# Kernel optimization log

Measured on AMD Instinct MI355X. Metric: run time of the kernel, lower is better.

## Reference

```python
import jax, jax.numpy as jnp
import numpy as np

B = 8192       # atmospheric columns (batch)
NLAY = 60      # vertical levels (RNN sequence length)
NX = 4         # per-level input features
NXS = 3        # surface scalar inputs
NH1 = 64       # rnn1 hidden
NH2 = 64       # rnn2 hidden
NMEM = 16      # latent memory width (nh_mem)
NY = 4         # per-level outputs
NYS = 3        # surface outputs


def _lstm(x, h0, c0, Wih, Whh, bih, bhh):
    """PyTorch-convention LSTM (gate order i,f,g,o). x: [B,T,nx] -> ([B,T,nh], hL, cL)."""
    b = bih + bhh
    WihT = Wih.T
    WhhT = Whh.T

    def step(carry, xt):
        h, c = carry
        g = xt @ WihT + h @ WhhT + b
        i, f, gg, o = jnp.split(g, 4, axis=-1)
        c = jax.nn.sigmoid(f) * c + jax.nn.sigmoid(i) * jnp.tanh(gg)
        h = jax.nn.sigmoid(o) * jnp.tanh(c)
        return (h, c), h

    (hL, cL), ys = jax.lax.scan(step, (h0, c0), jnp.swapaxes(x, 0, 1))
    return jnp.swapaxes(ys, 0, 1), hL, cL


def setup_inputs() -> dict:
    key = jax.random.key(0)
    ks = jax.random.split(key, 30)

    def p(i, shape):
        return jax.random.normal(ks[i], shape, jnp.float32) * 0.05

    return {
        "inputs_main": jax.random.normal(ks[0], (B, NLAY, NX), jnp.float32),
        "inputs_aux": jax.random.normal(ks[1], (B, NXS), jnp.float32),
        "rnn1_mem": jax.random.normal(ks[2], (B, NLAY, NMEM), jnp.float32),
        # mlp_initial: Linear(nx, nneur[0])
        "Wi": p(3, (NH1, NX)), "bi": p(4, (NH1,)),
        # mlp_surface1/2: Linear(nx_sfc, nh_rnn1)
        "Ws1": p(5, (NH1, NXS)), "bs1": p(6, (NH1,)),
        "Ws2": p(7, (NH1, NXS)), "bs2": p(8, (NH1,)),
        # mlp_toa1/2: Linear(1, nh_rnn2)
        "Wt1": p(9, (NH2, 1)), "bt1": p(10, (NH2,)),
        "Wt2": p(11, (NH2, 1)), "bt2": p(12, (NH2,)),
        # rnn1: LSTM(NH1+NMEM -> NH1)
        "Wih1": p(13, (4 * NH1, NH1 + NMEM)), "Whh1": p(14, (4 * NH1, NH1)),
        "bih1": p(15, (4 * NH1,)), "bhh1": p(16, (4 * NH1,)),
        # rnn2: LSTM(NH1 -> NH2)
        "Wih2": p(17, (4 * NH2, NH1)), "Whh2": p(18, (4 * NH2, NH2)),
        "bih2": p(19, (4 * NH2,)), "bhh2": p(20, (4 * NH2,)),
        # mlp_latent: Linear(NH2, NMEM)
        "Wl": p(21, (NMEM, NH2)), "bl": p(22, (NMEM,)),
        # mlp_output: Linear(NMEM, NY)
        "Wo": p(23, (NY, NMEM)), "bo": p(24, (NY,)),
        # mlp_surface_output: Linear(NH2, NYS)
        "Wso": p(25, (NYS, NH2)), "bso": p(26, (NYS,)),
    }


def reference(inputs_main, inputs_aux, rnn1_mem, Wi, bi, Ws1, bs1, Ws2, bs2,
              Wt1, bt1, Wt2, bt2, Wih1, Whh1, bih1, bhh1, Wih2, Whh2, bih2, bhh2,
              Wl, bl, Wo, bo, Wso, bso):
    # initial MLP + tanh
    x = jnp.tanh(inputs_main @ Wi.T + bi)                       # [B,L,NH1]
    # concat convective memory
    x = jnp.concatenate([x, rnn1_mem], axis=2)                  # [B,L,NH1+NMEM]
    # rnn1 runs surface->TOA: flip level axis
    x = jnp.flip(x, axis=1)
    hx = jnp.tanh(inputs_aux @ Ws1.T + bs1)                     # surface-conditioned h0
    cx = jnp.tanh(inputs_aux @ Ws2.T + bs2)
    r1, _, _ = _lstm(x, hx, cx, Wih1, Whh1, bih1, bhh1)
    r1 = jnp.flip(r1, axis=1)                                   # back to TOA->surface
    # rnn2 initialized from TOA scalar
    toa = inputs_aux[:, 1:2]
    hx2 = toa @ Wt1.T + bt1
    cx2 = toa @ Wt2.T + bt2
    r2, hL, _ = _lstm(r1, hx2, cx2, Wih2, Whh2, bih2, bhh2)     # [B,L,NH2]
    # intermediate latent MLP -> new per-level memory
    lat = r2 @ Wl.T + bl                                        # [B,L,NMEM]
    new_mem = lat
    out = lat @ Wo.T + bo                                       # [B,L,NY]
    out_sfc = hL @ Wso.T + bso                                  # [B,NYS]
    return (out, out_sfc, new_mem)
```

## Files before the change

kernel.cpp:

```cpp
#include <hip/hip_runtime.h>
#include <hip/hip_bf16.h>

#define BATCH 8192
#define NLAY  60
#define NH    64
#define NMEM  16
#define ROWS  16
#define TPB   256
#define S1    168
#define S2    136

typedef unsigned short ushort_t;
typedef __attribute__((ext_vector_type(8))) short short8;
typedef __attribute__((ext_vector_type(4))) short short4v;
typedef __attribute__((ext_vector_type(4))) float f32x4;
typedef __attribute__((ext_vector_type(4))) float f4v;

__device__ __forceinline__ float rcp_(float x) { return __builtin_amdgcn_rcpf(x); }
__device__ __forceinline__ float sigm_(float x) { return rcp_(1.0f + __expf(-x)); }
__device__ __forceinline__ float tanh_(float x) { return 1.0f - 2.0f * rcp_(__expf(2.0f * x) + 1.0f); }
__device__ __forceinline__ ushort_t f2bu(float f) {
  unsigned u = __float_as_uint(f);
  return (ushort_t)((u + 0x7FFFu + ((u >> 16) & 1u)) >> 16);
}
__device__ __forceinline__ float b2fu(ushort_t b) { return __uint_as_float(((unsigned)b) << 16); }

__device__ __forceinline__ f32x4 mfma16(short8 a, short8 b, f32x4 c) {
  return __builtin_amdgcn_mfma_f32_16x16x32_bf16(a, b, c, 0, 0, 0);
}

__global__ void wtranspose(const float* __restrict__ Wih1, const float* __restrict__ Whh1,
                           const float* __restrict__ Wih2, const float* __restrict__ Whh2,
                           const float* __restrict__ Wl, ushort_t* __restrict__ frag) {
  int e = blockIdx.x * 256 + threadIdx.x;
  float v;
  if (e < 40960) {
    int j = e & 7, lx = (e >> 3) & 63, rest = e >> 9;
    int ks = rest % 5, gw = rest / 5;
    int g = gw & 3, wv = gw >> 2;
    int uu = wv * 16 + (lx & 15);
    int k = ks * 32 + (lx >> 4) * 8 + j;
    int row = g * 64 + uu;
    v = (k < 80) ? Wih1[row * 80 + k] : (k < 144 ? Whh1[row * 64 + (k - 80)] : 0.0f);
  } else if (e < 73728) {
    int e2 = e - 40960;
    int j = e2 & 7, lx = (e2 >> 3) & 63, rest = e2 >> 9;
    int ks = rest & 3, g = (rest >> 2) & 3, wv = rest >> 4;
    int uu = wv * 16 + (lx & 15);
    int k = ks * 32 + (lx >> 4) * 8 + j;
    int row = g * 64 + uu;
    v = (k < 64) ? Wih2[row * 64 + k] : Whh2[row * 64 + (k - 64)];
  } else {
    int e3 = e - 73728;
    int j = e3 & 7, lx = (e3 >> 3) & 63, ks = e3 >> 9;
    int m = lx & 15, k = ks * 32 + (lx >> 4) * 8 + j;
    v = Wl[m * 64 + k];
  }
  frag[e] = f2bu(v);
}

__global__ __launch_bounds__(TPB, 2)
void lstm_fused(const float* __restrict__ inputs_main, const float* __restrict__ inputs_aux,
                const float* __restrict__ rnn1_mem,
                const float* __restrict__ Wi,  const float* __restrict__ bi,
                const float* __restrict__ Ws1, const float* __restrict__ bs1,
                const float* __restrict__ Ws2, const float* __restrict__ bs2,
                const float* __restrict__ Wt1, const float* __restrict__ bt1,
                const float* __restrict__ Wt2, const float* __restrict__ bt2,
                const float* __restrict__ bih1, const float* __restrict__ bhh1,
                const float* __restrict__ bih2, const float* __restrict__ bhh2,
                const float* __restrict__ bl,
                const ushort_t* __restrict__ W1f, const ushort_t* __restrict__ W2f,
                const ushort_t* __restrict__ Wlf_g,
                ushort_t* __restrict__ r1buf, ushort_t* __restrict__ hLbuf,
                float* __restrict__ new_mem) {
  __shared__ __align__(16) ushort_t xh1[16 * S1];
  __shared__ __align__(16) ushort_t xh2[16 * S2];
  __shared__ __align__(16) float inmS[16][244];

  const int tid = threadIdx.x;
  const int l  = tid & 63, w = tid >> 6;
  const int ln = l & 15,  lq = l >> 4;
  const int u  = w * 16 + ln;
  const int rowbase = lq * 4;
  const int b0 = blockIdx.x * ROWS;
  const int xr = tid >> 4, xm = tid & 15, xc0 = xm * 4;
  const int rr8 = tid >> 3, ch8 = tid & 7;

  short8 B1f[4][5];
#pragma unroll
  for (int g = 0; g < 4; ++g)
#pragma unroll
    for (int ks = 0; ks < 5; ++ks)
      B1f[g][ks] = *(const short8*)(W1f + (((w * 4 + g) * 5 + ks) << 9) + (l << 3));

  f4v wif[4];
#pragma unroll
  for (int cc = 0; cc < 4; ++cc) wif[cc] = *(const f4v*)(Wi + (xc0 + cc) * 4);
  f4v bifv = *(const f4v*)(bi + xc0);

  float bg1[4];
#pragma unroll
  for (int g = 0; g < 4; ++g) bg1[g] = bih1[g * 64 + u] + bhh1[g * 64 + u];

  for (int e = tid; e < 16 * 240; e += TPB) {
    int r = e / 240, c = e - r * 240;
    inmS[r][c] = inputs_main[(size_t)(b0 + r) * 240 + c];
  }
  if (tid < 192) {
    int r = tid / 12, cc2 = (tid - r * 12) * 2 + 144;
    xh1[r * S1 + cc2] = 0; xh1[r * S1 + cc2 + 1] = 0;
  }
  __syncthreads();

  float c1[4];
  {
    float mv = rnn1_mem[(size_t)(b0 + xr) * 960 + 59 * 16 + xm];
    xh1[xr * S1 + 64 + xm] = f2bu(mv);
    f4v xin = *(const f4v*)&inmS[xr][59 * 4];
    short4v xpv;
#pragma unroll
    for (int cc = 0; cc < 4; ++cc) {
      float a = bifv[cc] + wif[cc][0] * xin[0] + wif[cc][1] * xin[1] + wif[cc][2] * xin[2] + wif[cc][3] * xin[3];
      xpv[cc] = (short)f2bu(tanh_(a));
    }
    *(short4v*)&xh1[xr * S1 + xc0] = xpv;

    float w10 = Ws1[u * 3 + 0], w11 = Ws1[u * 3 + 1], w12 = Ws1[u * 3 + 2], bb1 = bs1[u];
    float w20 = Ws2[u * 3 + 0], w21 = Ws2[u * 3 + 1], w22 = Ws2[u * 3 + 2], bb2 = bs2[u];
#pragma unroll
    for (int reg = 0; reg < 4; ++reg) {
      int row = rowbase + reg;
      const float* ax = inputs_aux + (size_t)(b0 + row) * 3;
      float a0 = ax[0], a1 = ax[1], a2 = ax[2];
      xh1[row * S1 + 80 + u] = f2bu(tanh_(w10 * a0 + w11 * a1 + w12 * a2 + bb1));
      c1[reg] = tanh_(w20 * a0 + w21 * a1 + w22 * a2 + bb2);
    }
  }
  __syncthreads();

  for (int t = NLAY - 1; t >= 0; --t) {
    float mv = 0.0f; f4v xin = {};
    if (t > 0) {
      mv  = rnn1_mem[(size_t)(b0 + xr) * 960 + (t - 1) * 16 + xm];
      xin = *(const f4v*)&inmS[xr][(t - 1) * 4];
    }
    short8 af[5];
#pragma unroll
    for (int ks = 0; ks < 5; ++ks)
      af[ks] = *(const short8*)&xh1[ln * S1 + ks * 32 + lq * 8];
    short4v hv = {};
    if (t < 59) hv = *(const short4v*)&xh1[xr * S1 + 80 + xc0];

    f32x4 acc[4];
#pragma unroll
    for (int g = 0; g < 4; ++g) acc[g] = (f32x4){bg1[g], bg1[g], bg1[g], bg1[g]};
#pragma unroll
    for (int ks = 0; ks < 5; ++ks)
#pragma unroll
      for (int g = 0; g < 4; ++g) acc[g] = mfma16(af[ks], B1f[g][ks], acc[g]);

    if (t < 59)
      *(short4v*)(r1buf + ((size_t)(b0 + xr) * 60 + (t + 1)) * 64 + xc0) = hv;

    short4v xpv = {};
    if (t > 0) {
#pragma unroll
      for (int cc = 0; cc < 4; ++cc) {
        float a = bifv[cc] + wif[cc][0] * xin[0] + wif[cc][1] * xin[1] + wif[cc][2] * xin[2] + wif[cc][3] * xin[3];
        xpv[cc] = (short)f2bu(tanh_(a));
      }
    }
    ushort_t hu[4];
#pragma unroll
    for (int reg = 0; reg < 4; ++reg) {
      float ig = sigm_(acc[0][reg]);
      float fg = sigm_(acc[1][reg]);
      float gg = tanh_(acc[2][reg]);
      float og = sigm_(acc[3][reg]);
      float c  = fg * c1[reg] + ig * gg;
      c1[reg] = c;
      hu[reg] = f2bu(og * tanh_(c));
    }
    __syncthreads();
#pragma unroll
    for (int reg = 0; reg < 4; ++reg) xh1[(rowbase + reg) * S1 + 80 + u] = hu[reg];
    if (t > 0) {
      *(short4v*)&xh1[xr * S1 + xc0] = xpv;
      xh1[xr * S1 + 64 + xm] = f2bu(mv);
    }
    __syncthreads();
  }

  float c2[4], bg2[4], blv;
  short8 B2f[4][4], Wlf[2];
  {
    short4v hv = *(const short4v*)&xh1[xr * S1 + 80 + xc0];
    *(short4v*)(r1buf + ((size_t)(b0 + xr) * 60 + 0) * 64 + xc0) = hv;
    *(short4v*)&xh2[xr * S2 + xc0] = hv;

    float wt1u = Wt1[u], wt2u = Wt2[u], bt1u = bt1[u], bt2u = bt2[u];
#pragma unroll
    for (int reg = 0; reg < 4; ++reg) {
      int row = rowbase + reg;
      float toa = inputs_aux[(size_t)(b0 + row) * 3 + 1];
      xh2[row * S2 + 64 + u] = f2bu(toa * wt1u + bt1u);
      c2[reg] = toa * wt2u + bt2u;
    }
#pragma unroll
    for (int g = 0; g < 4; ++g) bg2[g] = bih2[g * 64 + u] + bhh2[g * 64 + u];
#pragma unroll
    for (int g = 0; g < 4; ++g)
#pragma unroll
      for (int ks = 0; ks < 4; ++ks)
        B2f[g][ks] = *(const short8*)(W2f + (((w * 4 + g) * 4 + ks) << 9) + (l << 3));
    Wlf[0] = *(const short8*)(Wlf_g + (l << 3));
    Wlf[1] = *(const short8*)(Wlf_g + 512 + (l << 3));
    blv = bl[ln];
  }
  __syncthreads();

  for (int t = 0; t < NLAY; ++t) {
    short8 r1v = {};
    if (t < 59 && tid < 128)
      r1v = *(const short8*)(r1buf + ((size_t)(b0 + rr8) * 60 + (t + 1)) * 64 + ch8 * 8);
    short8 af2[4];
#pragma unroll
    for (int ks = 0; ks < 4; ++ks)
      af2[ks] = *(const short8*)&xh2[ln * S2 + ks * 32 + lq * 8];

    f32x4 acc[4];
#pragma unroll
    for (int g = 0; g < 4; ++g) acc[g] = (f32x4){bg2[g], bg2[g], bg2[g], bg2[g]};
#pragma unroll
    for (int ks = 0; ks < 4; ++ks)
#pragma unroll
      for (int g = 0; g < 4; ++g) acc[g] = mfma16(af2[ks], B2f[g][ks], acc[g]);

    ushort_t h2u[4];
#pragma unroll
    for (int reg = 0; reg < 4; ++reg) {
      float ig = sigm_(acc[0][reg]);
      float fg = sigm_(acc[1][reg]);
      float gg = tanh_(acc[2][reg]);
      float og = sigm_(acc[3][reg]);
      float c  = fg * c2[reg] + ig * gg;
      c2[reg] = c;
      h2u[reg] = f2bu(og * tanh_(c));
    }
    __syncthreads();
#pragma unroll
    for (int reg = 0; reg < 4; ++reg) xh2[(rowbase + reg) * S2 + 64 + u] = h2u[reg];
    if (t < 59 && tid < 128)
      *(short8*)&xh2[rr8 * S2 + ch8 * 8] = r1v;
    __syncthreads();

    if (w == 0) {
      short8 afL0 = *(const short8*)&xh2[ln * S2 + 64 + lq * 8];
      short8 afL1 = *(const short8*)&xh2[ln * S2 + 64 + 32 + lq * 8];
      f32x4 accL = (f32x4){blv, blv, blv, blv};
      accL = mfma16(afL0, Wlf[0], accL);
      accL = mfma16(afL1, Wlf[1], accL);
#pragma unroll
      for (int reg = 0; reg < 4; ++reg)
        new_mem[((size_t)(b0 + rowbase + reg) * 60 + t) * 16 + ln] = accL[reg];
    }
  }

  {
    short4v hv = *(const short4v*)&xh2[xr * S2 + 64 + xc0];
    *(short4v*)(hLbuf + (size_t)(b0 + xr) * 64 + xc0) = hv;
  }
}

__global__ void postpass(const float* __restrict__ new_mem, const ushort_t* __restrict__ hLbuf,
                         const float* __restrict__ Wo, const float* __restrict__ bo,
                         const float* __restrict__ Wso, const float* __restrict__ bso,
                         float* __restrict__ out, float* __restrict__ out_sfc) {
  int idx = blockIdx.x * 256 + threadIdx.x;
  int b = idx / 60, t = idx - b * 60;
  f4v nm[4];
#pragma unroll
  for (int i = 0; i < 4; ++i) nm[i] = *(const f4v*)(new_mem + (size_t)idx * 16 + i * 4);
  f4v ov;
#pragma unroll
  for (int y = 0; y < 4; ++y) {
    float a = bo[y];
#pragma unroll
    for (int m = 0; m < 16; ++m) a += nm[m >> 2][m & 3] * Wo[y * 16 + m];
    ov[y] = a;
  }
  *(f4v*)(out + (size_t)idx * 4) = ov;

  if (t == 59) {
    const ushort_t* hp = hLbuf + (size_t)b * 64;
    float s0 = bso[0], s1 = bso[1], s2 = bso[2];
#pragma unroll
    for (int kk = 0; kk < 8; ++kk) {
      short8 v = *(const short8*)(hp + kk * 8);
#pragma unroll
      for (int j = 0; j < 8; ++j) {
        float h = b2fu((ushort_t)v[j]);
        int k = kk * 8 + j;
        s0 += h * Wso[0 * 64 + k];
        s1 += h * Wso[1 * 64 + k];
        s2 += h * Wso[2 * 64 + k];
      }
    }
    out_sfc[(size_t)b * 3 + 0] = s0;
    out_sfc[(size_t)b * 3 + 1] = s1;
    out_sfc[(size_t)b * 3 + 2] = s2;
  }
}

extern "C" void kernel_launch(void* const* d_in, const int* in_sizes, int n_in,
                              void* d_out, int out_size, void* d_ws, size_t ws_size,
                              hipStream_t stream) {
  (void)in_sizes; (void)n_in; (void)out_size; (void)ws_size;
  const float* inputs_main = (const float*)d_in[0];
  const float* inputs_aux  = (const float*)d_in[1];
  const float* rnn1_mem    = (const float*)d_in[2];
  const float* Wi   = (const float*)d_in[3];
  const float* bi   = (const float*)d_in[4];
  const float* Ws1  = (const float*)d_in[5];
  const float* bs1  = (const float*)d_in[6];
  const float* Ws2  = (const float*)d_in[7];
  const float* bs2  = (const float*)d_in[8];
  const float* Wt1  = (const float*)d_in[9];
  const float* bt1  = (const float*)d_in[10];
  const float* Wt2  = (const float*)d_in[11];
  const float* bt2  = (const float*)d_in[12];
  const float* Wih1 = (const float*)d_in[13];
  const float* Whh1 = (const float*)d_in[14];
  const float* bih1 = (const float*)d_in[15];
  const float* bhh1 = (const float*)d_in[16];
  const float* Wih2 = (const float*)d_in[17];
  const float* Whh2 = (const float*)d_in[18];
  const float* bih2 = (const float*)d_in[19];
  const float* bhh2 = (const float*)d_in[20];
  const float* Wl   = (const float*)d_in[21];
  const float* bl   = (const float*)d_in[22];
  const float* Wo   = (const float*)d_in[23];
  const float* bo   = (const float*)d_in[24];
  const float* Wso  = (const float*)d_in[25];
  const float* bso  = (const float*)d_in[26];

  float* out     = (float*)d_out;
  float* out_sfc = out + (size_t)BATCH * NLAY * 4;
  float* new_mem = out_sfc + (size_t)BATCH * 3;

  ushort_t* frag  = (ushort_t*)d_ws;
  ushort_t* r1buf = (ushort_t*)((char*)d_ws + 149504);
  ushort_t* hLbuf = (ushort_t*)((char*)d_ws + 149504 + (size_t)BATCH * NLAY * NH * 2);

  wtranspose<<<292, 256, 0, stream>>>(Wih1, Whh1, Wih2, Whh2, Wl, frag);
  lstm_fused<<<BATCH / ROWS, TPB, 0, stream>>>(
      inputs_main, inputs_aux, rnn1_mem, Wi, bi, Ws1, bs1, Ws2, bs2,
      Wt1, bt1, Wt2, bt2, bih1, bhh1, bih2, bhh2, bl,
      frag, frag + 40960, frag + 73728, r1buf, hLbuf, new_mem);
  postpass<<<BATCH * NLAY / 256, 256, 0, stream>>>(new_mem, hLbuf, Wo, bo, Wso, bso, out, out_sfc);
}
```

Measured before the change: 279.9 us.

## Fuse output projections into LSTM kernel and double-buffer hidden state in LDS

Removes the postpass kernel. The output projection is folded algebraically into the latent weights (Wo·Wl) and computed with MFMA by a second wave, the surface output is computed by a third wave, and both run inside the rnn2 loop, one timestep behind. The xh1 and xh2 LDS buffers are double-buffered, which drops one __syncthreads per timestep. rnn1 now writes r1buf directly from the computed h rather than reading it back. In exchange LDS use grows and the per-step MFMA work is larger, and folding Wo into Wl before rounding to bf16 changes numerics slightly.

```diff
diff --git a/kernel.cpp b/kernel.cpp
--- a/kernel.cpp
+++ b/kernel.cpp
@@ -4,7 +4,6 @@
 #define BATCH 8192
 #define NLAY  60
 #define NH    64
-#define NMEM  16
 #define ROWS  16
 #define TPB   256
 #define S1    168
@@ -12,7 +11,6 @@
 
 typedef unsigned short ushort_t;
 typedef __attribute__((ext_vector_type(8))) short short8;
-typedef __attribute__((ext_vector_type(4))) short short4v;
 typedef __attribute__((ext_vector_type(4))) float f32x4;
 typedef __attribute__((ext_vector_type(4))) float f4v;
 
@@ -23,15 +21,19 @@
   unsigned u = __float_as_uint(f);
   return (ushort_t)((u + 0x7FFFu + ((u >> 16) & 1u)) >> 16);
 }
-__device__ __forceinline__ float b2fu(ushort_t b) { return __uint_as_float(((unsigned)b) << 16); }
-
+__device__ __forceinline__ unsigned pkbf(float a, float b) {
+  union { __hip_bfloat162 h; unsigned u; } c;
+  c.h = __float22bfloat162_rn(make_float2(a, b));
+  return c.u;
+}
 __device__ __forceinline__ f32x4 mfma16(short8 a, short8 b, f32x4 c) {
   return __builtin_amdgcn_mfma_f32_16x16x32_bf16(a, b, c, 0, 0, 0);
 }
 
 __global__ void wtranspose(const float* __restrict__ Wih1, const float* __restrict__ Whh1,
                            const float* __restrict__ Wih2, const float* __restrict__ Whh2,
-                           const float* __restrict__ Wl, ushort_t* __restrict__ frag) {
+                           const float* __restrict__ Wl,   const float* __restrict__ Wo,
+                           const float* __restrict__ Wso,  ushort_t* __restrict__ frag) {
   int e = blockIdx.x * 256 + threadIdx.x;
   float v;
   if (e < 40960) {
@@ -50,11 +52,25 @@
     int k = ks * 32 + (lx >> 4) * 8 + j;
     int row = g * 64 + uu;
     v = (k < 64) ? Wih2[row * 64 + k] : Whh2[row * 64 + (k - 64)];
-  } else {
+  } else if (e < 74752) {
     int e3 = e - 73728;
     int j = e3 & 7, lx = (e3 >> 3) & 63, ks = e3 >> 9;
-    int m = lx & 15, k = ks * 32 + (lx >> 4) * 8 + j;
-    v = Wl[m * 64 + k];
+    int n = lx & 15, k = ks * 32 + (lx >> 4) * 8 + j;
+    v = Wl[n * 64 + k];
+  } else if (e < 75776) {
+    int e4 = e - 74752;
+    int j = e4 & 7, lx = (e4 >> 3) & 63, ks = e4 >> 9;
+    int n = lx & 15, k = ks * 32 + (lx >> 4) * 8 + j;
+    v = 0.0f;
+    if (n < 4) {
+#pragma unroll
+      for (int m = 0; m < 16; ++m) v += Wo[n * 16 + m] * Wl[m * 64 + k];
+    }
+  } else {
+    int e5 = e - 75776;
+    int j = e5 & 7, lx = (e5 >> 3) & 63, ks = e5 >> 9;
+    int n = lx & 15, k = ks * 32 + (lx >> 4) * 8 + j;
+    v = (n < 3) ? Wso[n * 64 + k] : 0.0f;
   }
   frag[e] = f2bu(v);
 }
@@ -69,13 +85,20 @@
                 const float* __restrict__ Wt2, const float* __restrict__ bt2,
                 const float* __restrict__ bih1, const float* __restrict__ bhh1,
                 const float* __restrict__ bih2, const float* __restrict__ bhh2,
-                const float* __restrict__ bl,
-                const ushort_t* __restrict__ W1f, const ushort_t* __restrict__ W2f,
-                const ushort_t* __restrict__ Wlf_g,
-                ushort_t* __restrict__ r1buf, ushort_t* __restrict__ hLbuf,
+                const float* __restrict__ bl,  const float* __restrict__ Wo,
+                const float* __restrict__ bo,  const float* __restrict__ bso,
+                const ushort_t* __restrict__ frag,
+                ushort_t* __restrict__ r1buf,
+                float* __restrict__ out, float* __restrict__ out_sfc,
                 float* __restrict__ new_mem) {
-  __shared__ __align__(16) ushort_t xh1[16 * S1];
-  __shared__ __align__(16) ushort_t xh2[16 * S2];
+  const ushort_t* W1f = frag;
+  const ushort_t* W2f = frag + 40960;
+  const ushort_t* WlF = frag + 73728;
+  const ushort_t* WcF = frag + 74752;
+  const ushort_t* WsF = frag + 75776;
+
+  __shared__ __align__(16) ushort_t xh1[2][16 * S1];
+  __shared__ __align__(16) ushort_t xh2[2][16 * S2];
   __shared__ __align__(16) float inmS[16][244];
 
   const int tid = threadIdx.x;
@@ -107,24 +130,22 @@
     int r = e / 240, c = e - r * 240;
     inmS[r][c] = inputs_main[(size_t)(b0 + r) * 240 + c];
   }
-  if (tid < 192) {
-    int r = tid / 12, cc2 = (tid - r * 12) * 2 + 144;
-    xh1[r * S1 + cc2] = 0; xh1[r * S1 + cc2 + 1] = 0;
+  {
+    int r = tid >> 4, c = 144 + (tid & 15);
+    xh1[0][r * S1 + c] = 0; xh1[1][r * S1 + c] = 0;
   }
   __syncthreads();
 
   float c1[4];
   {
     float mv = rnn1_mem[(size_t)(b0 + xr) * 960 + 59 * 16 + xm];
-    xh1[xr * S1 + 64 + xm] = f2bu(mv);
+    xh1[0][xr * S1 + 64 + xm] = f2bu(mv);
     f4v xin = *(const f4v*)&inmS[xr][59 * 4];
-    short4v xpv;
-#pragma unroll
-    for (int cc = 0; cc < 4; ++cc) {
-      float a = bifv[cc] + wif[cc][0] * xin[0] + wif[cc][1] * xin[1] + wif[cc][2] * xin[2] + wif[cc][3] * xin[3];
-      xpv[cc] = (short)f2bu(tanh_(a));
-    }
-    *(short4v*)&xh1[xr * S1 + xc0] = xpv;
+    float xp[4];
+#pragma unroll
+    for (int cc = 0; cc < 4; ++cc)
+      xp[cc] = tanh_(bifv[cc] + wif[cc][0]*xin[0] + wif[cc][1]*xin[1] + wif[cc][2]*xin[2] + wif[cc][3]*xin[3]);
+    *(uint2*)&xh1[0][xr * S1 + xc0] = make_uint2(pkbf(xp[0], xp[1]), pkbf(xp[2], xp[3]));
 
     float w10 = Ws1[u * 3 + 0], w11 = Ws1[u * 3 + 1], w12 = Ws1[u * 3 + 2], bb1 = bs1[u];
     float w20 = Ws2[u * 3 + 0], w21 = Ws2[u * 3 + 1], w22 = Ws2[u * 3 + 2], bb2 = bs2[u];
@@ -133,13 +154,15 @@
       int row = rowbase + reg;
       const float* ax = inputs_aux + (size_t)(b0 + row) * 3;
       float a0 = ax[0], a1 = ax[1], a2 = ax[2];
-      xh1[row * S1 + 80 + u] = f2bu(tanh_(w10 * a0 + w11 * a1 + w12 * a2 + bb1));
+      xh1[0][row * S1 + 80 + u] = f2bu(tanh_(w10 * a0 + w11 * a1 + w12 * a2 + bb1));
       c1[reg] = tanh_(w20 * a0 + w21 * a1 + w22 * a2 + bb2);
     }
   }
   __syncthreads();
 
+  int pb = 0;
   for (int t = NLAY - 1; t >= 0; --t) {
+    const int nb = pb ^ 1;
     float mv = 0.0f; f4v xin = {};
     if (t > 0) {
       mv  = rnn1_mem[(size_t)(b0 + xr) * 960 + (t - 1) * 16 + xm];
@@ -148,9 +171,7 @@
     short8 af[5];
 #pragma unroll
     for (int ks = 0; ks < 5; ++ks)
-      af[ks] = *(const short8*)&xh1[ln * S1 + ks * 32 + lq * 8];
-    short4v hv = {};
-    if (t < 59) hv = *(const short4v*)&xh1[xr * S1 + 80 + xc0];
+      af[ks] = *(const short8*)&xh1[pb][ln * S1 + ks * 32 + lq * 8];
 
     f32x4 acc[4];
 #pragma unroll
@@ -160,18 +181,16 @@
 #pragma unroll
       for (int g = 0; g < 4; ++g) acc[g] = mfma16(af[ks], B1f[g][ks], acc[g]);
 
-    if (t < 59)
-      *(short4v*)(r1buf + ((size_t)(b0 + xr) * 60 + (t + 1)) * 64 + xc0) = hv;
-
-    short4v xpv = {};
     if (t > 0) {
-#pragma unroll
-      for (int cc = 0; cc < 4; ++cc) {
-        float a = bifv[cc] + wif[cc][0] * xin[0] + wif[cc][1] * xin[1] + wif[cc][2] * xin[2] + wif[cc][3] * xin[3];
-        xpv[cc] = (short)f2bu(tanh_(a));
-      }
-    }
-    ushort_t hu[4];
+      float xp[4];
+#pragma unroll
+      for (int cc = 0; cc < 4; ++cc)
+        xp[cc] = tanh_(bifv[cc] + wif[cc][0]*xin[0] + wif[cc][1]*xin[1] + wif[cc][2]*xin[2] + wif[cc][3]*xin[3]);
+      *(uint2*)&xh1[nb][xr * S1 + xc0] = make_uint2(pkbf(xp[0], xp[1]), pkbf(xp[2], xp[3]));
+      xh1[nb][xr * S1 + 64 + xm] = f2bu(mv);
+    }
+
+    float h[4];
 #pragma unroll
     for (int reg = 0; reg < 4; ++reg) {
       float ig = sigm_(acc[0][reg]);
@@ -180,54 +199,73 @@
       float og = sigm_(acc[3][reg]);
       float c  = fg * c1[reg] + ig * gg;
       c1[reg] = c;
-      hu[reg] = f2bu(og * tanh_(c));
+      h[reg] = og * tanh_(c);
+    }
+    unsigned h01 = pkbf(h[0], h[1]), h23 = pkbf(h[2], h[3]);
+    ushort_t hu[4] = {(ushort_t)h01, (ushort_t)(h01 >> 16), (ushort_t)h23, (ushort_t)(h23 >> 16)};
+#pragma unroll
+    for (int reg = 0; reg < 4; ++reg) {
+      r1buf[((size_t)(b0 + rowbase + reg) * 60 + t) * 64 + u] = hu[reg];
+      if (t > 0) xh1[nb][(rowbase + reg) * S1 + 80 + u] = hu[reg];
+      else       xh2[0][(rowbase + reg) * S2 + u]       = hu[reg];
     }
     __syncthreads();
-#pragma unroll
-    for (int reg = 0; reg < 4; ++reg) xh1[(rowbase + reg) * S1 + 80 + u] = hu[reg];
-    if (t > 0) {
-      *(short4v*)&xh1[xr * S1 + xc0] = xpv;
-      xh1[xr * S1 + 64 + xm] = f2bu(mv);
-    }
-    __syncthreads();
-  }
-
-  float c2[4], bg2[4], blv;
-  short8 B2f[4][4], Wlf[2];
+    pb = nb;
+  }
+
+  short8 B2f[4][4];
+#pragma unroll
+  for (int g = 0; g < 4; ++g)
+#pragma unroll
+    for (int ks = 0; ks < 4; ++ks)
+      B2f[g][ks] = *(const short8*)(W2f + (((w * 4 + g) * 4 + ks) << 9) + (l << 3));
+  float bg2[4];
+#pragma unroll
+  for (int g = 0; g < 4; ++g) bg2[g] = bih2[g * 64 + u] + bhh2[g * 64 + u];
+
+  float c2[4];
   {
-    short4v hv = *(const short4v*)&xh1[xr * S1 + 80 + xc0];
-    *(short4v*)(r1buf + ((size_t)(b0 + xr) * 60 + 0) * 64 + xc0) = hv;
-    *(short4v*)&xh2[xr * S2 + xc0] = hv;
-
     float wt1u = Wt1[u], wt2u = Wt2[u], bt1u = bt1[u], bt2u = bt2[u];
 #pragma unroll
     for (int reg = 0; reg < 4; ++reg) {
       int row = rowbase + reg;
       float toa = inputs_aux[(size_t)(b0 + row) * 3 + 1];
-      xh2[row * S2 + 64 + u] = f2bu(toa * wt1u + bt1u);
+      xh2[0][row * S2 + 64 + u] = f2bu(toa * wt1u + bt1u);
       c2[reg] = toa * wt2u + bt2u;
     }
-#pragma unroll
-    for (int g = 0; g < 4; ++g) bg2[g] = bih2[g * 64 + u] + bhh2[g * 64 + u];
-#pragma unroll
-    for (int g = 0; g < 4; ++g)
-#pragma unroll
-      for (int ks = 0; ks < 4; ++ks)
-        B2f[g][ks] = *(const short8*)(W2f + (((w * 4 + g) * 4 + ks) << 9) + (l << 3));
-    Wlf[0] = *(const short8*)(Wlf_g + (l << 3));
-    Wlf[1] = *(const short8*)(Wlf_g + 512 + (l << 3));
-    blv = bl[ln];
+  }
+  short8 PW0 = {}, PW1 = {};
+  float pbias = 0.0f;
+  if (w == 0) {
+    PW0 = *(const short8*)(WlF + (l << 3));
+    PW1 = *(const short8*)(WlF + 512 + (l << 3));
+    pbias = bl[ln];
+  } else if (w == 1) {
+    PW0 = *(const short8*)(WcF + (l << 3));
+    PW1 = *(const short8*)(WcF + 512 + (l << 3));
+    if (ln < 4) {
+      float a = bo[ln];
+#pragma unroll
+      for (int m = 0; m < 16; ++m) a += Wo[ln * 16 + m] * bl[m];
+      pbias = a;
+    }
+  } else if (w == 2) {
+    PW0 = *(const short8*)(WsF + (l << 3));
+    PW1 = *(const short8*)(WsF + 512 + (l << 3));
+    pbias = (ln < 3) ? bso[ln] : 0.0f;
   }
   __syncthreads();
 
+  pb = 0;
   for (int t = 0; t < NLAY; ++t) {
+    const int nb = pb ^ 1;
     short8 r1v = {};
     if (t < 59 && tid < 128)
       r1v = *(const short8*)(r1buf + ((size_t)(b0 + rr8) * 60 + (t + 1)) * 64 + ch8 * 8);
     short8 af2[4];
 #pragma unroll
     for (int ks = 0; ks < 4; ++ks)
-      af2[ks] = *(const short8*)&xh2[ln * S2 + ks * 32 + lq * 8];
+      af2[ks] = *(const short8*)&xh2[pb][ln * S2 + ks * 32 + lq * 8];
 
     f32x4 acc[4];
 #pragma unroll
@@ -237,7 +275,24 @@
 #pragma unroll
       for (int g = 0; g < 4; ++g) acc[g] = mfma16(af2[ks], B2f[g][ks], acc[g]);
 
-    ushort_t h2u[4];
+    if (t > 0 && w < 2) {
+      short8 aL0 = *(const short8*)&xh2[pb][ln * S2 + 64 + lq * 8];
+      short8 aL1 = *(const short8*)&xh2[pb][ln * S2 + 96 + lq * 8];
+      f32x4 ap = (f32x4){pbias, pbias, pbias, pbias};
+      ap = mfma16(aL0, PW0, ap);
+      ap = mfma16(aL1, PW1, ap);
+      if (w == 0) {
+#pragma unroll
+        for (int reg = 0; reg < 4; ++reg)
+          new_mem[((size_t)(b0 + rowbase + reg) * 60 + (t - 1)) * 16 + ln] = ap[reg];
+      } else if (ln < 4) {
+#pragma unroll
+        for (int reg = 0; reg < 4; ++reg)
+          out[((size_t)(b0 + rowbase + reg) * 60 + (t - 1)) * 4 + ln] = ap[reg];
+      }
+    }
+
+    float h[4];
 #pragma unroll
     for (int reg = 0; reg < 4; ++reg) {
       float ig = sigm_(acc[0][reg]);
@@ -246,70 +301,42 @@
       float og = sigm_(acc[3][reg]);
       float c  = fg * c2[reg] + ig * gg;
       c2[reg] = c;
-      h2u[reg] = f2bu(og * tanh_(c));
-    }
+      h[reg] = og * tanh_(c);
+    }
+    unsigned h01 = pkbf(h[0], h[1]), h23 = pkbf(h[2], h[3]);
+    ushort_t hu[4] = {(ushort_t)h01, (ushort_t)(h01 >> 16), (ushort_t)h23, (ushort_t)(h23 >> 16)};
+#pragma unroll
+    for (int reg = 0; reg < 4; ++reg)
+      xh2[nb][(rowbase + reg) * S2 + 64 + u] = hu[reg];
+    if (t < 59 && tid < 128)
+      *(short8*)&xh2[nb][rr8 * S2 + ch8 * 8] = r1v;
     __syncthreads();
-#pragma unroll
-    for (int reg = 0; reg < 4; ++reg) xh2[(rowbase + reg) * S2 + 64 + u] = h2u[reg];
-    if (t < 59 && tid < 128)
-      *(short8*)&xh2[rr8 * S2 + ch8 * 8] = r1v;
-    __syncthreads();
-
+    pb = nb;
+  }
+
+  if (w < 3) {
+    short8 aL0 = *(const short8*)&xh2[0][ln * S2 + 64 + lq * 8];
+    short8 aL1 = *(const short8*)&xh2[0][ln * S2 + 96 + lq * 8];
+    f32x4 ap = (f32x4){pbias, pbias, pbias, pbias};
+    ap = mfma16(aL0, PW0, ap);
+    ap = mfma16(aL1, PW1, ap);
     if (w == 0) {
-      short8 afL0 = *(const short8*)&xh2[ln * S2 + 64 + lq * 8];
-      short8 afL1 = *(const short8*)&xh2[ln * S2 + 64 + 32 + lq * 8];
-      f32x4 accL = (f32x4){blv, blv, blv, blv};
-      accL = mfma16(afL0, Wlf[0], accL);
-      accL = mfma16(afL1, Wlf[1], accL);
 #pragma unroll
       for (int reg = 0; reg < 4; ++reg)
-        new_mem[((size_t)(b0 + rowbase + reg) * 60 + t) * 16 + ln] = accL[reg];
-    }
-  }
-
-  {
-    short4v hv = *(const short4v*)&xh2[xr * S2 + 64 + xc0];
-    *(short4v*)(hLbuf + (size_t)(b0 + xr) * 64 + xc0) = hv;
-  }
-}
-
-__global__ void postpass(const float* __restrict__ new_mem, const ushort_t* __restrict__ hLbuf,
-                         const float* __restrict__ Wo, const float* __restrict__ bo,
-                         const float* __restrict__ Wso, const float* __restrict__ bso,
-                         float* __restrict__ out, float* __restrict__ out_sfc) {
-  int idx = blockIdx.x * 256 + threadIdx.x;
-  int b = idx / 60, t = idx - b * 60;
-  f4v nm[4];
-#pragma unroll
-  for (int i = 0; i < 4; ++i) nm[i] = *(const f4v*)(new_mem + (size_t)idx * 16 + i * 4);
-  f4v ov;
-#pragma unroll
-  for (int y = 0; y < 4; ++y) {
-    float a = bo[y];
-#pragma unroll
-    for (int m = 0; m < 16; ++m) a += nm[m >> 2][m & 3] * Wo[y * 16 + m];
-    ov[y] = a;
-  }
-  *(f4v*)(out + (size_t)idx * 4) = ov;
-
-  if (t == 59) {
-    const ushort_t* hp = hLbuf + (size_t)b * 64;
-    float s0 = bso[0], s1 = bso[1], s2 = bso[2];
-#pragma unroll
-    for (int kk = 0; kk < 8; ++kk) {
-      short8 v = *(const short8*)(hp + kk * 8);
-#pragma unroll
-      for (int j = 0; j < 8; ++j) {
-        float h = b2fu((ushort_t)v[j]);
-        int k = kk * 8 + j;
-        s0 += h * Wso[0 * 64 + k];
-        s1 += h * Wso[1 * 64 + k];
-        s2 += h * Wso[2 * 64 + k];
+        new_mem[((size_t)(b0 + rowbase + reg) * 60 + 59) * 16 + ln] = ap[reg];
+    } else if (w == 1) {
+      if (ln < 4) {
+#pragma unroll
+        for (int reg = 0; reg < 4; ++reg)
+          out[((size_t)(b0 + rowbase + reg) * 60 + 59) * 4 + ln] = ap[reg];
       }
-    }
-    out_sfc[(size_t)b * 3 + 0] = s0;
-    out_sfc[(size_t)b * 3 + 1] = s1;
-    out_sfc[(size_t)b * 3 + 2] = s2;
+    } else {
+      if (ln < 3) {
+#pragma unroll
+        for (int reg = 0; reg < 4; ++reg)
+          out_sfc[(size_t)(b0 + rowbase + reg) * 3 + ln] = ap[reg];
+      }
+    }
   }
 }
 
@@ -350,13 +377,11 @@
   float* new_mem = out_sfc + (size_t)BATCH * 3;
 
   ushort_t* frag  = (ushort_t*)d_ws;
-  ushort_t* r1buf = (ushort_t*)((char*)d_ws + 149504);
-  ushort_t* hLbuf = (ushort_t*)((char*)d_ws + 149504 + (size_t)BATCH * NLAY * NH * 2);
-
-  wtranspose<<<292, 256, 0, stream>>>(Wih1, Whh1, Wih2, Whh2, Wl, frag);
+  ushort_t* r1buf = (ushort_t*)((char*)d_ws + 153600);
+
+  wtranspose<<<300, 256, 0, stream>>>(Wih1, Whh1, Wih2, Whh2, Wl, Wo, Wso, frag);
   lstm_fused<<<BATCH / ROWS, TPB, 0, stream>>>(
       inputs_main, inputs_aux, rnn1_mem, Wi, bi, Ws1, bs1, Ws2, bs2,
-      Wt1, bt1, Wt2, bt2, bih1, bhh1, bih2, bhh2, bl,
-      frag, frag + 40960, frag + 73728, r1buf, hLbuf, new_mem);
-  postpass<<<BATCH * NLAY / 256, 256, 0, stream>>>(new_mem, hLbuf, Wo, bo, Wso, bso, out, out_sfc);
-}
+      Wt1, bt1, Wt2, bt2, bih1, bhh1, bih2, bhh2, bl, Wo, bo, bso,
+      frag, r1buf, out, out_sfc, new_mem);
+}
```

Result: faster. 263.5 us (-5.8%).
